# Optimization experiments

Measured on AMD Instinct MI355X. Metric: run time of the kernel, lower is better.

## Reference

```python
import jax, jax.numpy as jnp
import numpy as np

N_NODES = 100000
N_EDGES = 800000
IN_F, H_F, OUT_F = 512, 256, 64
N_EXPERTS = 4  # k = 1


def _normalize_edges(edge_index, n):
    """gcn_norm: add self loops, symmetric D^-1/2 A D^-1/2 edge weights."""
    loop = jnp.arange(n, dtype=edge_index.dtype)
    row = jnp.concatenate([edge_index[0], loop])
    col = jnp.concatenate([edge_index[1], loop])
    w = jnp.ones(row.shape[0], dtype=jnp.float32)
    deg = jax.ops.segment_sum(w, col, num_segments=n)  # in-degree incl. self loop
    dinv = jnp.where(deg > 0, deg ** -0.5, 0.0)
    norm = dinv[row] * w * dinv[col]
    return row, col, norm


def _propagate(x, row, col, norm, n):
    # message x_j * edge_weight, scatter-add at destination col
    msgs = x[row] * norm[:, None]
    return jax.ops.segment_sum(msgs, col, num_segments=n)


def _moe_linear(x, w_gate, expert_w, expert_b):
    # eval-mode noisy top-k gating with k=1: clean logits, top-1, softmax over
    # a single logit -> gate value 1.0 for the selected expert.
    logits = x @ w_gate                         # [N, E]
    idx = jnp.argmax(logits, axis=-1)           # [N]
    gates = jax.nn.one_hot(idx, N_EXPERTS, dtype=x.dtype)  # [N, E]
    y_all = jnp.einsum('ni,eio->neo', x, expert_w) + expert_b[None]  # [N, E, H]
    return jnp.einsum('ne,neo->no', gates, y_all)


def setup_inputs() -> dict:
    key = jax.random.key(0)
    ks = jax.random.split(key, 8)
    x = jax.random.normal(ks[0], (N_NODES, IN_F), dtype=jnp.float32)
    edge_index = jax.random.randint(ks[1], (2, N_EDGES), 0, N_NODES, dtype=jnp.int64)
    w_gate = jax.random.normal(ks[2], (IN_F, N_EXPERTS), dtype=jnp.float32) * 0.05
    expert_w = jax.random.normal(ks[3], (N_EXPERTS, IN_F, H_F), dtype=jnp.float32) * (1.0 / np.sqrt(IN_F))
    expert_b = jnp.zeros((N_EXPERTS, H_F), dtype=jnp.float32)
    bias1 = jnp.zeros((H_F,), dtype=jnp.float32)
    w2 = jax.random.normal(ks[4], (H_F, OUT_F), dtype=jnp.float32) * (1.0 / np.sqrt(H_F))
    bias2 = jnp.zeros((OUT_F,), dtype=jnp.float32)
    return {"x": x, "edge_index": edge_index, "w_gate": w_gate,
            "expert_w": expert_w, "expert_b": expert_b, "bias1": bias1,
            "w2": w2, "bias2": bias2}


def reference(x, edge_index, w_gate, expert_w, expert_b, bias1, w2, bias2):
    n = x.shape[0]
    row, col, norm = _normalize_edges(edge_index, n)
    # conv1: MoE linear -> propagate -> bias
    h = _moe_linear(x, w_gate, expert_w, expert_b)
    h = _propagate(h, row, col, norm, n) + bias1
    h = jax.nn.relu(h)
    # dropout is identity at eval
    # conv2: plain GCNConv
    h = h @ w2
    h = _propagate(h, row, col, norm, n) + bias2
    return jax.nn.log_softmax(h, axis=1)
```

## Files before the change

kernel.cpp:

```cpp
#include <hip/hip_runtime.h>
#include <math.h>

typedef __bf16 bf16x8 __attribute__((ext_vector_type(8)));
typedef float f32x16 __attribute__((ext_vector_type(16)));

__device__ __forceinline__ unsigned short f2bf(float f) {
  union { float f; unsigned int u; } v; v.f = f;
  unsigned int r = (v.u + 0x7FFFu + ((v.u >> 16) & 1u)) >> 16;
  return (unsigned short)r;
}
__device__ __forceinline__ float bf2f(unsigned short u) {
  union { unsigned int u; float f; } v; v.u = ((unsigned int)u) << 16;
  return v.f;
}
__device__ __forceinline__ void bf2x(unsigned int u, float& lo, float& hi) {
  union { unsigned int u; float f; } a, b;
  a.u = u << 16; b.u = u & 0xFFFF0000u;
  lo = a.f; hi = b.f;
}
__device__ __forceinline__ void gload16(const void* g, void* l) {
  __builtin_amdgcn_global_load_lds(
      (__attribute__((address_space(1))) void*)const_cast<void*>(g),
      (__attribute__((address_space(3))) void*)l, 16, 0, 0);
}

__global__ void k_init(int* cnt, int* meta, int N) {
  int i = blockIdx.x * blockDim.x + threadIdx.x;
  if (i < N) cnt[i] = 0;
  if (i < 32) meta[i] = 0;
}

__global__ void k_count(const int* __restrict__ col, int* __restrict__ cnt, int E) {
  int e = blockIdx.x * blockDim.x + threadIdx.x;
  if (e < E) atomicAdd(&cnt[col[e]], 1);
}

__global__ __launch_bounds__(256) void k_scanA(const int* __restrict__ cnt,
                                               int* __restrict__ incl,
                                               int* __restrict__ bsums, int N) {
  __shared__ int s[1024];
  int base = blockIdx.x * 1024;
  #pragma unroll
  for (int t = 0; t < 4; ++t) {
    int i = threadIdx.x + t * 256;
    int idx = base + i;
    s[i] = (idx < N) ? cnt[idx] : 0;
  }
  __syncthreads();
  for (int d = 1; d < 1024; d <<= 1) {
    int v[4];
    #pragma unroll
    for (int t = 0; t < 4; ++t) {
      int i = threadIdx.x + t * 256;
      v[t] = (i >= d) ? s[i - d] : 0;
    }
    __syncthreads();
    #pragma unroll
    for (int t = 0; t < 4; ++t) {
      int i = threadIdx.x + t * 256;
      s[i] += v[t];
    }
    __syncthreads();
  }
  #pragma unroll
  for (int t = 0; t < 4; ++t) {
    int i = threadIdx.x + t * 256;
    int idx = base + i;
    if (idx < N) incl[idx] = s[i];
  }
  if (threadIdx.x == 0) bsums[blockIdx.x] = s[1023];
}

__global__ __launch_bounds__(256) void k_scanB(const int* __restrict__ bsums,
                                               int* __restrict__ boff, int nb) {
  __shared__ int s[1024];
  #pragma unroll
  for (int t = 0; t < 4; ++t) {
    int i = threadIdx.x + t * 256;
    s[i] = (i < nb) ? bsums[i] : 0;
  }
  __syncthreads();
  for (int d = 1; d < 1024; d <<= 1) {
    int v[4];
    #pragma unroll
    for (int t = 0; t < 4; ++t) {
      int i = threadIdx.x + t * 256;
      v[t] = (i >= d) ? s[i - d] : 0;
    }
    __syncthreads();
    #pragma unroll
    for (int t = 0; t < 4; ++t) {
      int i = threadIdx.x + t * 256;
      s[i] += v[t];
    }
    __syncthreads();
  }
  #pragma unroll
  for (int t = 0; t < 4; ++t) {
    int i = threadIdx.x + t * 256;
    if (i < nb) boff[i] = (i == 0) ? 0 : s[i - 1];
  }
}

__global__ void k_scanC(const int* __restrict__ cnt, const int* __restrict__ incl,
                        const int* __restrict__ boff, int* __restrict__ rowptr,
                        int* __restrict__ cursor, float* __restrict__ dinv, int N, int E) {
  int i = blockIdx.x * blockDim.x + threadIdx.x;
  if (i < N) {
    int ex = incl[i] - cnt[i] + boff[i >> 10];
    rowptr[i] = ex;
    cursor[i] = ex;
    dinv[i] = rsqrtf((float)(cnt[i] + 1));
    if (i == 0) rowptr[N] = E;
  }
}

__global__ void k_scatter(const int* __restrict__ row, const int* __restrict__ col,
                          int* __restrict__ cursor, int* __restrict__ csr, int E) {
  int e = blockIdx.x * blockDim.x + threadIdx.x;
  if (e < E) {
    int c = col[e];
    int p = atomicAdd(&cursor[c], 1);
    csr[p] = row[e];
  }
}

__global__ __launch_bounds__(256) void k_gate(const float* __restrict__ x,
                                              const float* __restrict__ wg,
                                              int* __restrict__ eidx,
                                              int* __restrict__ meta,
                                              unsigned short* __restrict__ xb, int N) {
  __shared__ int lhist[4];
  int tid = threadIdx.x;
  if (tid < 4) lhist[tid] = 0;
  __syncthreads();
  int node = blockIdx.x * 16 + (tid >> 4);
  int sl = tid & 15;
  if (node < N) {
    const float* xr = x + (size_t)node * 512;
    unsigned short* xbr = xb + (size_t)node * 512;
    float l0 = 0.f, l1 = 0.f, l2 = 0.f, l3 = 0.f;
    #pragma unroll
    for (int j = 0; j < 8; ++j) {
      int q = sl + 16 * j;
      float4 xv = *(const float4*)(xr + 4 * q);
      ushort4 ov;
      ov.x = f2bf(xv.x); ov.y = f2bf(xv.y); ov.z = f2bf(xv.z); ov.w = f2bf(xv.w);
      *(ushort4*)(xbr + 4 * q) = ov;
      float4 w0 = *(const float4*)(wg + 4 * (4 * q + 0));
      float4 w1 = *(const float4*)(wg + 4 * (4 * q + 1));
      float4 w2 = *(const float4*)(wg + 4 * (4 * q + 2));
      float4 w3 = *(const float4*)(wg + 4 * (4 * q + 3));
      l0 += xv.x * w0.x + xv.y * w1.x + xv.z * w2.x + xv.w * w3.x;
      l1 += xv.x * w0.y + xv.y * w1.y + xv.z * w2.y + xv.w * w3.y;
      l2 += xv.x * w0.z + xv.y * w1.z + xv.z * w2.z + xv.w * w3.z;
      l3 += xv.x * w0.w + xv.y * w1.w + xv.z * w2.w + xv.w * w3.w;
    }
    #pragma unroll
    for (int off = 8; off > 0; off >>= 1) {
      l0 += __shfl_xor(l0, off, 64);
      l1 += __shfl_xor(l1, off, 64);
      l2 += __shfl_xor(l2, off, 64);
      l3 += __shfl_xor(l3, off, 64);
    }
    if (sl == 0) {
      int a = 0; float best = l0;
      if (l1 > best) { best = l1; a = 1; }
      if (l2 > best) { best = l2; a = 2; }
      if (l3 > best) { best = l3; a = 3; }
      eidx[node] = a;
      atomicAdd(&lhist[a], 1);
    }
  }
  __syncthreads();
  if (tid < 4 && lhist[tid] > 0) atomicAdd(&meta[tid], lhist[tid]);
}

__global__ void k_offs(int* meta) {
  if (threadIdx.x == 0 && blockIdx.x == 0) {
    int* hist = meta;
    int* eoff = meta + 4;
    int* toff = meta + 9;
    int* ecur = meta + 14;
    int s = 0, t = 0;
    eoff[0] = 0; toff[0] = 0;
    for (int e = 0; e < 4; ++e) {
      s += hist[e];
      eoff[e + 1] = s;
      t += (hist[e] + 127) / 128;
      toff[e + 1] = t;
      ecur[e] = eoff[e];
    }
  }
}

__global__ __launch_bounds__(256) void k_binscatter(const int* __restrict__ eidx,
                                                    int* __restrict__ meta,
                                                    int* __restrict__ perm, int N) {
  __shared__ int lhist[4];
  __shared__ int lbase[4];
  int tid = threadIdx.x;
  if (tid < 4) lhist[tid] = 0;
  __syncthreads();
  int n = blockIdx.x * 256 + tid;
  int e = 0, lrank = 0;
  bool valid = (n < N);
  if (valid) {
    e = eidx[n];
    lrank = atomicAdd(&lhist[e], 1);
  }
  __syncthreads();
  if (tid < 4) {
    int c = lhist[tid];
    lbase[tid] = (c > 0) ? atomicAdd(&meta[14 + tid], c) : 0;
  }
  __syncthreads();
  if (valid) perm[lbase[e] + lrank] = n;
}

__global__ __launch_bounds__(256) void k_pack(const float* __restrict__ ew,
                                              unsigned short* __restrict__ ewb,
                                              const float* __restrict__ w2,
                                              unsigned short* __restrict__ w2b) {
  int b = blockIdx.x;
  if (b < 256) {
    int n = threadIdx.x;
    int e = b >> 6, kc = b & 63;
    const float* src = ew + ((size_t)e * 512 + (size_t)kc * 8) * 256 + n;
    unsigned short tmp[8];
    #pragma unroll
    for (int ke = 0; ke < 8; ++ke) tmp[ke] = f2bf(src[(size_t)ke * 256]);
    *(uint4*)(ewb + ((size_t)b * 256 + n) * 8) = *(const uint4*)tmp;
  } else {
    int kc = b - 256;
    int n = threadIdx.x;
    if (n < 64) {
      const float* src = w2 + (size_t)kc * 8 * 64 + n;
      unsigned short tmp[8];
      #pragma unroll
      for (int ke = 0; ke < 8; ++ke) tmp[ke] = f2bf(src[(size_t)ke * 64]);
      *(uint4*)(w2b + ((size_t)kc * 64 + n) * 8) = *(const uint4*)tmp;
    }
  }
}

__global__ __launch_bounds__(512, 2) void k_gemm1(const unsigned short* __restrict__ xb,
                                                  const unsigned short* __restrict__ ewb,
                                                  const float* __restrict__ eb,
                                                  const int* __restrict__ perm,
                                                  const int* __restrict__ meta,
                                                  unsigned short* __restrict__ h1) {
  __shared__ __align__(16) unsigned short A_lds[8192];
  __shared__ __align__(16) unsigned short B_lds[16384];
  __shared__ int sperm[128];
  const int* eoff = meta + 4;
  const int* toff = meta + 9;
  int v = blockIdx.x;
  if (v >= toff[4]) return;
  int e = 0;
  while (v >= toff[e + 1]) ++e;
  int m0 = eoff[e] + (v - toff[e]) * 128;
  int mEnd = eoff[e + 1];
  int tid = threadIdx.x;

  if (tid < 128) {
    int m = m0 + tid;
    sperm[tid] = perm[(m < mEnd) ? m : (mEnd - 1)];
  }
  __syncthreads();

  int wave = tid >> 6, lane = tid & 63;
  int wr = wave >> 2, wc = wave & 3;
  int hi = lane >> 5, lo = lane & 31;
  int r128 = tid & 127;

  f32x16 acc[2][2];
  #pragma unroll
  for (int mi = 0; mi < 2; ++mi)
    #pragma unroll
    for (int ni = 0; ni < 2; ++ni)
      #pragma unroll
      for (int r = 0; r < 16; ++r) acc[mi][ni][r] = 0.f;

  const unsigned short* arow = xb + (size_t)sperm[r128] * 512;
  int kclA = tid >> 7;
  const uint4* ebase = (const uint4*)(ewb + (size_t)e * 64 * 2048);

  for (int k0 = 0; k0 < 512; k0 += 64) {
    __syncthreads();
    gload16(arow + k0 + kclA * 8,       &A_lds[((size_t)kclA * 128 + r128) * 8]);
    gload16(arow + k0 + (kclA + 4) * 8, &A_lds[((size_t)(kclA + 4) * 128 + r128) * 8]);
    const uint4* bsrc = ebase + (size_t)(k0 >> 3) * 256;
    gload16(bsrc + tid,        &B_lds[((size_t)0 * 512 + tid) * 8]);
    gload16(bsrc + 512 + tid,  &B_lds[((size_t)1 * 512 + tid) * 8]);
    gload16(bsrc + 1024 + tid, &B_lds[((size_t)2 * 512 + tid) * 8]);
    gload16(bsrc + 1536 + tid, &B_lds[((size_t)3 * 512 + tid) * 8]);
    __syncthreads();
    #pragma unroll
    for (int s = 0; s < 4; ++s) {
      int kcl = s * 2 + hi;
      bf16x8 a0f = *(const bf16x8*)&A_lds[((size_t)kcl * 128 + wr * 64 + lo) * 8];
      bf16x8 a1f = *(const bf16x8*)&A_lds[((size_t)kcl * 128 + wr * 64 + 32 + lo) * 8];
      bf16x8 b0f = *(const bf16x8*)&B_lds[((size_t)kcl * 256 + wc * 64 + lo) * 8];
      bf16x8 b1f = *(const bf16x8*)&B_lds[((size_t)kcl * 256 + wc * 64 + 32 + lo) * 8];
      acc[0][0] = __builtin_amdgcn_mfma_f32_32x32x16_bf16(a0f, b0f, acc[0][0], 0, 0, 0);
      acc[0][1] = __builtin_amdgcn_mfma_f32_32x32x16_bf16(a0f, b1f, acc[0][1], 0, 0, 0);
      acc[1][0] = __builtin_amdgcn_mfma_f32_32x32x16_bf16(a1f, b0f, acc[1][0], 0, 0, 0);
      acc[1][1] = __builtin_amdgcn_mfma_f32_32x32x16_bf16(a1f, b1f, acc[1][1], 0, 0, 0);
    }
  }

  #pragma unroll
  for (int ni = 0; ni < 2; ++ni) {
    int col = wc * 64 + ni * 32 + lo;
    float bias = eb[e * 256 + col];
    #pragma unroll
    for (int mi = 0; mi < 2; ++mi) {
      #pragma unroll
      for (int q = 0; q < 4; ++q) {
        #pragma unroll
        for (int j = 0; j < 4; ++j) {
          int r = j + 8 * q + 4 * hi;
          int lrow = wr * 64 + mi * 32 + r;
          if (m0 + lrow < mEnd) {
            h1[(size_t)sperm[lrow] * 256 + col] = f2bf(acc[mi][ni][q * 4 + j] + bias);
          }
        }
      }
    }
  }
}

__global__ __launch_bounds__(256) void k_prop1(const unsigned short* __restrict__ h1,
                                               const int* __restrict__ rowptr,
                                               const int* __restrict__ csr,
                                               const float* __restrict__ dinv,
                                               const float* __restrict__ bias1,
                                               unsigned short* __restrict__ hrelu, int N) {
  int tid = threadIdx.x;
  int c = blockIdx.x * 8 + (tid >> 5);
  int l = tid & 31;
  if (c >= N) return;
  float dc = dinv[c];
  const uint4* hr = (const uint4*)h1;
  uint4 sv = hr[(size_t)c * 32 + l];
  float slf = dc * dc;
  float a0, a1, a2, a3, a4, a5, a6, a7;
  {
    float lo, hi;
    bf2x(sv.x, lo, hi); a0 = lo * slf; a1 = hi * slf;
    bf2x(sv.y, lo, hi); a2 = lo * slf; a3 = hi * slf;
    bf2x(sv.z, lo, hi); a4 = lo * slf; a5 = hi * slf;
    bf2x(sv.w, lo, hi); a6 = lo * slf; a7 = hi * slf;
  }
  int jb = rowptr[c], je = rowptr[c + 1];
  int j = jb;
  #define ACC8(v, s) { float lo, hi; \
    bf2x((v).x, lo, hi); a0 += lo * (s); a1 += hi * (s); \
    bf2x((v).y, lo, hi); a2 += lo * (s); a3 += hi * (s); \
    bf2x((v).z, lo, hi); a4 += lo * (s); a5 += hi * (s); \
    bf2x((v).w, lo, hi); a6 += lo * (s); a7 += hi * (s); }
  for (; j + 7 < je; j += 8) {
    int r[8];
    #pragma unroll
    for (int t = 0; t < 8; ++t) r[t] = csr[j + t];
    float s[8];
    #pragma unroll
    for (int t = 0; t < 8; ++t) s[t] = dinv[r[t]] * dc;
    uint4 vv[8];
    #pragma unroll
    for (int t = 0; t < 8; ++t) vv[t] = hr[(size_t)r[t] * 32 + l];
    #pragma unroll
    for (int t = 0; t < 8; ++t) ACC8(vv[t], s[t]);
  }
  for (; j + 3 < je; j += 4) {
    int r0 = csr[j], r1 = csr[j + 1], r2 = csr[j + 2], r3 = csr[j + 3];
    float s0 = dinv[r0] * dc, s1 = dinv[r1] * dc, s2 = dinv[r2] * dc, s3 = dinv[r3] * dc;
    uint4 v0 = hr[(size_t)r0 * 32 + l];
    uint4 v1 = hr[(size_t)r1 * 32 + l];
    uint4 v2 = hr[(size_t)r2 * 32 + l];
    uint4 v3 = hr[(size_t)r3 * 32 + l];
    ACC8(v0, s0); ACC8(v1, s1); ACC8(v2, s2); ACC8(v3, s3);
  }
  for (; j < je; ++j) {
    int r = csr[j];
    float s = dinv[r] * dc;
    uint4 v = hr[(size_t)r * 32 + l];
    ACC8(v, s);
  }
  #undef ACC8
  float4 b01 = *(const float4*)(bias1 + l * 8);
  float4 b23 = *(const float4*)(bias1 + l * 8 + 4);
  a0 = fmaxf(a0 + b01.x, 0.f); a1 = fmaxf(a1 + b01.y, 0.f);
  a2 = fmaxf(a2 + b01.z, 0.f); a3 = fmaxf(a3 + b01.w, 0.f);
  a4 = fmaxf(a4 + b23.x, 0.f); a5 = fmaxf(a5 + b23.y, 0.f);
  a6 = fmaxf(a6 + b23.z, 0.f); a7 = fmaxf(a7 + b23.w, 0.f);
  uint4 ov;
  ov.x = ((unsigned int)f2bf(a1) << 16) | f2bf(a0);
  ov.y = ((unsigned int)f2bf(a3) << 16) | f2bf(a2);
  ov.z = ((unsigned int)f2bf(a5) << 16) | f2bf(a4);
  ov.w = ((unsigned int)f2bf(a7) << 16) | f2bf(a6);
  ((uint4*)hrelu)[(size_t)c * 32 + l] = ov;
}

__global__ __launch_bounds__(256, 2) void k_gemm2(const unsigned short* __restrict__ A,
                                                  const unsigned short* __restrict__ w2b,
                                                  unsigned short* __restrict__ h3, int N) {
  __shared__ __align__(16) unsigned short B_lds[16384];
  __shared__ __align__(16) unsigned short A_lds[8192];
  int tid = threadIdx.x;
  int m0 = blockIdx.x * 128;
  #pragma unroll
  for (int it = 0; it < 8; ++it)
    gload16(((const uint4*)w2b) + it * 256 + tid, &B_lds[((size_t)it * 256 + tid) * 8]);

  int wave = tid >> 6, lane = tid & 63;
  int wr = wave >> 1, wc = wave & 1;
  int hi = lane >> 5, lo = lane & 31;

  f32x16 acc[2];
  #pragma unroll
  for (int mi = 0; mi < 2; ++mi)
    #pragma unroll
    for (int r = 0; r < 16; ++r) acc[mi][r] = 0.f;

  int i = tid & 127;
  int row = m0 + i;
  if (row >= N) row = N - 1;
  const unsigned short* arow = A + (size_t)row * 256;
  int kcl0 = tid >> 7;

  for (int k0 = 0; k0 < 256; k0 += 64) {
    __syncthreads();
    #pragma unroll
    for (int t = 0; t < 4; ++t)
      gload16(arow + k0 + (kcl0 + 2 * t) * 8,
              &A_lds[((size_t)(kcl0 + 2 * t) * 128 + i) * 8]);
    __syncthreads();
    #pragma unroll
    for (int s = 0; s < 4; ++s) {
      int kcl = s * 2 + hi;
      bf16x8 a0f = *(const bf16x8*)&A_lds[((size_t)kcl * 128 + wr * 64 + lo) * 8];
      bf16x8 a1f = *(const bf16x8*)&A_lds[((size_t)kcl * 128 + wr * 64 + 32 + lo) * 8];
      bf16x8 bf = *(const bf16x8*)&B_lds[(((size_t)(k0 >> 3) + kcl) * 64 + wc * 32 + lo) * 8];
      acc[0] = __builtin_amdgcn_mfma_f32_32x32x16_bf16(a0f, bf, acc[0], 0, 0, 0);
      acc[1] = __builtin_amdgcn_mfma_f32_32x32x16_bf16(a1f, bf, acc[1], 0, 0, 0);
    }
  }

  int n = wc * 32 + lo;
  #pragma unroll
  for (int mi = 0; mi < 2; ++mi) {
    #pragma unroll
    for (int q = 0; q < 4; ++q) {
      #pragma unroll
      for (int j = 0; j < 4; ++j) {
        int r = j + 8 * q + 4 * hi;
        int orow = m0 + wr * 64 + mi * 32 + r;
        if (orow < N) h3[(size_t)orow * 64 + n] = f2bf(acc[mi][q * 4 + j]);
      }
    }
  }
}

__global__ __launch_bounds__(256) void k_prop2(const unsigned short* __restrict__ h3,
                                               const int* __restrict__ rowptr,
                                               const int* __restrict__ csr,
                                               const float* __restrict__ dinv,
                                               const float* __restrict__ bias2,
                                               float* __restrict__ out, int N) {
  int tid = threadIdx.x;
  int c = blockIdx.x * 32 + (tid >> 3);
  int l = tid & 7;
  if (c >= N) return;
  float dc = dinv[c];
  const uint4* hr = (const uint4*)h3;
  uint4 sv = hr[(size_t)c * 8 + l];
  float slf = dc * dc;
  float a0, a1, a2, a3, a4, a5, a6, a7;
  {
    float lo, hi;
    bf2x(sv.x, lo, hi); a0 = lo * slf; a1 = hi * slf;
    bf2x(sv.y, lo, hi); a2 = lo * slf; a3 = hi * slf;
    bf2x(sv.z, lo, hi); a4 = lo * slf; a5 = hi * slf;
    bf2x(sv.w, lo, hi); a6 = lo * slf; a7 = hi * slf;
  }
  int jb = rowptr[c], je = rowptr[c + 1];
  int j = jb;
  #define ACC8(v, s) { float lo, hi; \
    bf2x((v).x, lo, hi); a0 += lo * (s); a1 += hi * (s); \
    bf2x((v).y, lo, hi); a2 += lo * (s); a3 += hi * (s); \
    bf2x((v).z, lo, hi); a4 += lo * (s); a5 += hi * (s); \
    bf2x((v).w, lo, hi); a6 += lo * (s); a7 += hi * (s); }
  for (; j + 7 < je; j += 8) {
    int r[8];
    #pragma unroll
    for (int t = 0; t < 8; ++t) r[t] = csr[j + t];
    float s[8];
    #pragma unroll
    for (int t = 0; t < 8; ++t) s[t] = dinv[r[t]] * dc;
    uint4 vv[8];
    #pragma unroll
    for (int t = 0; t < 8; ++t) vv[t] = hr[(size_t)r[t] * 8 + l];
    #pragma unroll
    for (int t = 0; t < 8; ++t) ACC8(vv[t], s[t]);
  }
  for (; j + 3 < je; j += 4) {
    int r0 = csr[j], r1 = csr[j + 1], r2 = csr[j + 2], r3 = csr[j + 3];
    float s0 = dinv[r0] * dc, s1 = dinv[r1] * dc, s2 = dinv[r2] * dc, s3 = dinv[r3] * dc;
    uint4 v0 = hr[(size_t)r0 * 8 + l];
    uint4 v1 = hr[(size_t)r1 * 8 + l];
    uint4 v2 = hr[(size_t)r2 * 8 + l];
    uint4 v3 = hr[(size_t)r3 * 8 + l];
    ACC8(v0, s0); ACC8(v1, s1); ACC8(v2, s2); ACC8(v3, s3);
  }
  for (; j < je; ++j) {
    int r = csr[j];
    float s = dinv[r] * dc;
    uint4 v = hr[(size_t)r * 8 + l];
    ACC8(v, s);
  }
  #undef ACC8
  float4 b01 = *(const float4*)(bias2 + l * 8);
  float4 b23 = *(const float4*)(bias2 + l * 8 + 4);
  a0 += b01.x; a1 += b01.y; a2 += b01.z; a3 += b01.w;
  a4 += b23.x; a5 += b23.y; a6 += b23.z; a7 += b23.w;
  float m = fmaxf(fmaxf(fmaxf(a0, a1), fmaxf(a2, a3)), fmaxf(fmaxf(a4, a5), fmaxf(a6, a7)));
  #pragma unroll
  for (int off = 4; off > 0; off >>= 1) m = fmaxf(m, __shfl_xor(m, off, 64));
  float s = expf(a0 - m) + expf(a1 - m) + expf(a2 - m) + expf(a3 - m)
          + expf(a4 - m) + expf(a5 - m) + expf(a6 - m) + expf(a7 - m);
  #pragma unroll
  for (int off = 4; off > 0; off >>= 1) s += __shfl_xor(s, off, 64);
  float ls = m + logf(s);
  float* orow = out + (size_t)c * 64 + l * 8;
  float4 o0 = make_float4(a0 - ls, a1 - ls, a2 - ls, a3 - ls);
  float4 o1 = make_float4(a4 - ls, a5 - ls, a6 - ls, a7 - ls);
  *(float4*)orow = o0;
  *(float4*)(orow + 4) = o1;
}

extern "C" void kernel_launch(void* const* d_in, const int* in_sizes, int n_in,
                              void* d_out, int out_size, void* d_ws, size_t ws_size,
                              hipStream_t stream) {
  const float* x  = (const float*)d_in[0];
  const int*   ei = (const int*)d_in[1];
  const float* wg = (const float*)d_in[2];
  const float* ew = (const float*)d_in[3];
  const float* eb = (const float*)d_in[4];
  const float* b1 = (const float*)d_in[5];
  const float* w2 = (const float*)d_in[6];
  const float* b2 = (const float*)d_in[7];
  float* out = (float*)d_out;

  int N = in_sizes[0] / 512;
  int E = in_sizes[1] / 2;
  const int* row = ei;
  const int* col = ei + E;

  char* p = (char*)d_ws;
  auto alloc = [&](size_t bytes) -> void* {
    void* r = (void*)p;
    p += (bytes + 255) & ~(size_t)255;
    return r;
  };
  int*   cnt    = (int*)alloc((size_t)N * 4);
  int*   rowptr = (int*)alloc((size_t)(N + 1) * 4);
  int*   cursor = (int*)alloc((size_t)N * 4);
  int*   bsums  = (int*)alloc(1024 * 4);
  int*   boff   = (int*)alloc(1024 * 4);
  float* dinv   = (float*)alloc((size_t)N * 4);
  int*   eidx   = (int*)alloc((size_t)N * 4);
  int*   meta   = (int*)alloc(32 * 4);
  int*   perm   = (int*)alloc((size_t)N * 4);
  int*   csr    = (int*)alloc((size_t)E * 4);
  unsigned short* h1    = (unsigned short*)alloc((size_t)N * 256 * 2);
  unsigned short* hrelu = (unsigned short*)alloc((size_t)N * 256 * 2);
  unsigned short* h3    = (unsigned short*)alloc((size_t)N * 64 * 2);
  unsigned short* xb  = (unsigned short*)alloc((size_t)N * 512 * 2);
  unsigned short* ewb = (unsigned short*)alloc((size_t)4 * 512 * 256 * 2);
  unsigned short* w2b = (unsigned short*)alloc((size_t)256 * 64 * 2);

  int nb = (N + 1023) / 1024;

  k_init<<<(N + 255) / 256, 256, 0, stream>>>(cnt, meta, N);
  k_count<<<(E + 255) / 256, 256, 0, stream>>>(col, cnt, E);
  k_scanA<<<nb, 256, 0, stream>>>(cnt, rowptr, bsums, N);
  k_scanB<<<1, 256, 0, stream>>>(bsums, boff, nb);
  k_scanC<<<(N + 255) / 256, 256, 0, stream>>>(cnt, rowptr, boff, rowptr, cursor, dinv, N, E);
  k_scatter<<<(E + 255) / 256, 256, 0, stream>>>(row, col, cursor, csr, E);
  k_pack<<<288, 256, 0, stream>>>(ew, ewb, w2, w2b);
  k_gate<<<(N + 15) / 16, 256, 0, stream>>>(x, wg, eidx, meta, xb, N);
  k_offs<<<1, 64, 0, stream>>>(meta);
  k_binscatter<<<(N + 255) / 256, 256, 0, stream>>>(eidx, meta, perm, N);
  int ntiles = (N + 127) / 128 + 4;
  k_gemm1<<<ntiles, 512, 0, stream>>>(xb, ewb, eb, perm, meta, h1);
  k_prop1<<<(N + 7) / 8, 256, 0, stream>>>(h1, rowptr, csr, dinv, b1, hrelu, N);
  k_gemm2<<<(N + 127) / 128, 256, 0, stream>>>(hrelu, w2b, h3, N);
  k_prop2<<<(N + 31) / 32, 256, 0, stream>>>(h3, rowptr, csr, dinv, b2, out, N);
}
```

Baseline: 397.3 us.

## Fuse count/pack into gate kernel and store source dinv alongside CSR indices

Merges the edge-count atomics and the weight-packing kernel into the gate kernel through block-index ranges, which removes two launches and lets the independent work run concurrently. The CSR now stores (row, dinv[row]) pairs, so the propagation kernels skip a dependent random gather of dinv per edge. In exchange the CSR array doubles in size, and the scatter kernel does an extra dinv gather per edge. The k_gate blocks that take the count and pack paths return before the shared-memory section, which may lengthen that kernel's tail.

```diff
diff --git a/kernel.cpp b/kernel.cpp
--- a/kernel.cpp
+++ b/kernel.cpp
@@ -28,11 +28,6 @@
   int i = blockIdx.x * blockDim.x + threadIdx.x;
   if (i < N) cnt[i] = 0;
   if (i < 32) meta[i] = 0;
-}
-
-__global__ void k_count(const int* __restrict__ col, int* __restrict__ cnt, int E) {
-  int e = blockIdx.x * blockDim.x + threadIdx.x;
-  if (e < E) atomicAdd(&cnt[col[e]], 1);
 }
 
 __global__ __launch_bounds__(256) void k_scanA(const int* __restrict__ cnt,
@@ -116,12 +111,14 @@
 }
 
 __global__ void k_scatter(const int* __restrict__ row, const int* __restrict__ col,
-                          int* __restrict__ cursor, int* __restrict__ csr, int E) {
+                          int* __restrict__ cursor, const float* __restrict__ dinv,
+                          int2* __restrict__ csr2, int E) {
   int e = blockIdx.x * blockDim.x + threadIdx.x;
   if (e < E) {
     int c = col[e];
+    int r = row[e];
     int p = atomicAdd(&cursor[c], 1);
-    csr[p] = row[e];
+    csr2[p] = make_int2(r, __float_as_int(dinv[r]));
   }
 }
 
@@ -129,9 +126,44 @@
                                               const float* __restrict__ wg,
                                               int* __restrict__ eidx,
                                               int* __restrict__ meta,
-                                              unsigned short* __restrict__ xb, int N) {
+                                              unsigned short* __restrict__ xb,
+                                              const int* __restrict__ col,
+                                              int* __restrict__ cnt,
+                                              const float* __restrict__ ew,
+                                              unsigned short* __restrict__ ewb,
+                                              const float* __restrict__ w2,
+                                              unsigned short* __restrict__ w2b,
+                                              int N, int E, int gateB, int cntB) {
+  int tid = threadIdx.x;
+  if (blockIdx.x >= (unsigned)gateB) {
+    int b = blockIdx.x - gateB;
+    if (b < cntB) {
+      int e = b * 256 + tid;
+      if (e < E) atomicAdd(&cnt[col[e]], 1);
+    } else {
+      b -= cntB;
+      if (b < 256) {
+        int n = tid;
+        int eidx2 = b >> 6, kc = b & 63;
+        const float* src = ew + ((size_t)eidx2 * 512 + (size_t)kc * 8) * 256 + n;
+        unsigned short tmp[8];
+        #pragma unroll
+        for (int ke = 0; ke < 8; ++ke) tmp[ke] = f2bf(src[(size_t)ke * 256]);
+        *(uint4*)(ewb + ((size_t)b * 256 + n) * 8) = *(const uint4*)tmp;
+      } else {
+        int kc = b - 256;
+        if (tid < 64) {
+          const float* src = w2 + (size_t)kc * 8 * 64 + tid;
+          unsigned short tmp[8];
+          #pragma unroll
+          for (int ke = 0; ke < 8; ++ke) tmp[ke] = f2bf(src[(size_t)ke * 64]);
+          *(uint4*)(w2b + ((size_t)kc * 64 + tid) * 8) = *(const uint4*)tmp;
+        }
+      }
+    }
+    return;
+  }
   __shared__ int lhist[4];
-  int tid = threadIdx.x;
   if (tid < 4) lhist[tid] = 0;
   __syncthreads();
   int node = blockIdx.x * 16 + (tid >> 4);
@@ -149,12 +181,12 @@
       *(ushort4*)(xbr + 4 * q) = ov;
       float4 w0 = *(const float4*)(wg + 4 * (4 * q + 0));
       float4 w1 = *(const float4*)(wg + 4 * (4 * q + 1));
-      float4 w2 = *(const float4*)(wg + 4 * (4 * q + 2));
+      float4 w2v = *(const float4*)(wg + 4 * (4 * q + 2));
       float4 w3 = *(const float4*)(wg + 4 * (4 * q + 3));
-      l0 += xv.x * w0.x + xv.y * w1.x + xv.z * w2.x + xv.w * w3.x;
-      l1 += xv.x * w0.y + xv.y * w1.y + xv.z * w2.y + xv.w * w3.y;
-      l2 += xv.x * w0.z + xv.y * w1.z + xv.z * w2.z + xv.w * w3.z;
-      l3 += xv.x * w0.w + xv.y * w1.w + xv.z * w2.w + xv.w * w3.w;
+      l0 += xv.x * w0.x + xv.y * w1.x + xv.z * w2v.x + xv.w * w3.x;
+      l1 += xv.x * w0.y + xv.y * w1.y + xv.z * w2v.y + xv.w * w3.y;
+      l2 += xv.x * w0.z + xv.y * w1.z + xv.z * w2v.z + xv.w * w3.z;
+      l3 += xv.x * w0.w + xv.y * w1.w + xv.z * w2v.w + xv.w * w3.w;
     }
     #pragma unroll
     for (int off = 8; off > 0; off >>= 1) {
@@ -216,32 +248,6 @@
   }
   __syncthreads();
   if (valid) perm[lbase[e] + lrank] = n;
-}
-
-__global__ __launch_bounds__(256) void k_pack(const float* __restrict__ ew,
-                                              unsigned short* __restrict__ ewb,
-                                              const float* __restrict__ w2,
-                                              unsigned short* __restrict__ w2b) {
-  int b = blockIdx.x;
-  if (b < 256) {
-    int n = threadIdx.x;
-    int e = b >> 6, kc = b & 63;
-    const float* src = ew + ((size_t)e * 512 + (size_t)kc * 8) * 256 + n;
-    unsigned short tmp[8];
-    #pragma unroll
-    for (int ke = 0; ke < 8; ++ke) tmp[ke] = f2bf(src[(size_t)ke * 256]);
-    *(uint4*)(ewb + ((size_t)b * 256 + n) * 8) = *(const uint4*)tmp;
-  } else {
-    int kc = b - 256;
-    int n = threadIdx.x;
-    if (n < 64) {
-      const float* src = w2 + (size_t)kc * 8 * 64 + n;
-      unsigned short tmp[8];
-      #pragma unroll
-      for (int ke = 0; ke < 8; ++ke) tmp[ke] = f2bf(src[(size_t)ke * 64]);
-      *(uint4*)(w2b + ((size_t)kc * 64 + n) * 8) = *(const uint4*)tmp;
-    }
-  }
 }
 
 __global__ __launch_bounds__(512, 2) void k_gemm1(const unsigned short* __restrict__ xb,
@@ -333,7 +339,7 @@
 
 __global__ __launch_bounds__(256) void k_prop1(const unsigned short* __restrict__ h1,
                                                const int* __restrict__ rowptr,
-                                               const int* __restrict__ csr,
+                                               const int2* __restrict__ csr2,
                                                const float* __restrict__ dinv,
                                                const float* __restrict__ bias1,
                                                unsigned short* __restrict__ hrelu, int N) {
@@ -361,31 +367,32 @@
     bf2x((v).z, lo, hi); a4 += lo * (s); a5 += hi * (s); \
     bf2x((v).w, lo, hi); a6 += lo * (s); a7 += hi * (s); }
   for (; j + 7 < je; j += 8) {
-    int r[8];
-    #pragma unroll
-    for (int t = 0; t < 8; ++t) r[t] = csr[j + t];
-    float s[8];
-    #pragma unroll
-    for (int t = 0; t < 8; ++t) s[t] = dinv[r[t]] * dc;
+    int2 rc[8];
+    #pragma unroll
+    for (int t = 0; t < 8; ++t) rc[t] = csr2[j + t];
     uint4 vv[8];
     #pragma unroll
-    for (int t = 0; t < 8; ++t) vv[t] = hr[(size_t)r[t] * 32 + l];
-    #pragma unroll
-    for (int t = 0; t < 8; ++t) ACC8(vv[t], s[t]);
+    for (int t = 0; t < 8; ++t) vv[t] = hr[(size_t)rc[t].x * 32 + l];
+    #pragma unroll
+    for (int t = 0; t < 8; ++t) {
+      float s = __int_as_float(rc[t].y) * dc;
+      ACC8(vv[t], s);
+    }
   }
   for (; j + 3 < je; j += 4) {
-    int r0 = csr[j], r1 = csr[j + 1], r2 = csr[j + 2], r3 = csr[j + 3];
-    float s0 = dinv[r0] * dc, s1 = dinv[r1] * dc, s2 = dinv[r2] * dc, s3 = dinv[r3] * dc;
-    uint4 v0 = hr[(size_t)r0 * 32 + l];
-    uint4 v1 = hr[(size_t)r1 * 32 + l];
-    uint4 v2 = hr[(size_t)r2 * 32 + l];
-    uint4 v3 = hr[(size_t)r3 * 32 + l];
+    int2 rc0 = csr2[j], rc1 = csr2[j + 1], rc2 = csr2[j + 2], rc3 = csr2[j + 3];
+    uint4 v0 = hr[(size_t)rc0.x * 32 + l];
+    uint4 v1 = hr[(size_t)rc1.x * 32 + l];
+    uint4 v2 = hr[(size_t)rc2.x * 32 + l];
+    uint4 v3 = hr[(size_t)rc3.x * 32 + l];
+    float s0 = __int_as_float(rc0.y) * dc, s1 = __int_as_float(rc1.y) * dc;
+    float s2 = __int_as_float(rc2.y) * dc, s3 = __int_as_float(rc3.y) * dc;
     ACC8(v0, s0); ACC8(v1, s1); ACC8(v2, s2); ACC8(v3, s3);
   }
   for (; j < je; ++j) {
-    int r = csr[j];
-    float s = dinv[r] * dc;
-    uint4 v = hr[(size_t)r * 32 + l];
+    int2 rc = csr2[j];
+    float s = __int_as_float(rc.y) * dc;
+    uint4 v = hr[(size_t)rc.x * 32 + l];
     ACC8(v, s);
   }
   #undef ACC8
@@ -465,7 +472,7 @@
 
 __global__ __launch_bounds__(256) void k_prop2(const unsigned short* __restrict__ h3,
                                                const int* __restrict__ rowptr,
-                                               const int* __restrict__ csr,
+                                               const int2* __restrict__ csr2,
                                                const float* __restrict__ dinv,
                                                const float* __restrict__ bias2,
                                                float* __restrict__ out, int N) {
@@ -493,31 +500,32 @@
     bf2x((v).z, lo, hi); a4 += lo * (s); a5 += hi * (s); \
     bf2x((v).w, lo, hi); a6 += lo * (s); a7 += hi * (s); }
   for (; j + 7 < je; j += 8) {
-    int r[8];
-    #pragma unroll
-    for (int t = 0; t < 8; ++t) r[t] = csr[j + t];
-    float s[8];
-    #pragma unroll
-    for (int t = 0; t < 8; ++t) s[t] = dinv[r[t]] * dc;
+    int2 rc[8];
+    #pragma unroll
+    for (int t = 0; t < 8; ++t) rc[t] = csr2[j + t];
     uint4 vv[8];
     #pragma unroll
-    for (int t = 0; t < 8; ++t) vv[t] = hr[(size_t)r[t] * 8 + l];
-    #pragma unroll
-    for (int t = 0; t < 8; ++t) ACC8(vv[t], s[t]);
+    for (int t = 0; t < 8; ++t) vv[t] = hr[(size_t)rc[t].x * 8 + l];
+    #pragma unroll
+    for (int t = 0; t < 8; ++t) {
+      float s = __int_as_float(rc[t].y) * dc;
+      ACC8(vv[t], s);
+    }
   }
   for (; j + 3 < je; j += 4) {
-    int r0 = csr[j], r1 = csr[j + 1], r2 = csr[j + 2], r3 = csr[j + 3];
-    float s0 = dinv[r0] * dc, s1 = dinv[r1] * dc, s2 = dinv[r2] * dc, s3 = dinv[r3] * dc;
-    uint4 v0 = hr[(size_t)r0 * 8 + l];
-    uint4 v1 = hr[(size_t)r1 * 8 + l];
-    uint4 v2 = hr[(size_t)r2 * 8 + l];
-    uint4 v3 = hr[(size_t)r3 * 8 + l];
+    int2 rc0 = csr2[j], rc1 = csr2[j + 1], rc2 = csr2[j + 2], rc3 = csr2[j + 3];
+    uint4 v0 = hr[(size_t)rc0.x * 8 + l];
+    uint4 v1 = hr[(size_t)rc1.x * 8 + l];
+    uint4 v2 = hr[(size_t)rc2.x * 8 + l];
+    uint4 v3 = hr[(size_t)rc3.x * 8 + l];
+    float s0 = __int_as_float(rc0.y) * dc, s1 = __int_as_float(rc1.y) * dc;
+    float s2 = __int_as_float(rc2.y) * dc, s3 = __int_as_float(rc3.y) * dc;
     ACC8(v0, s0); ACC8(v1, s1); ACC8(v2, s2); ACC8(v3, s3);
   }
   for (; j < je; ++j) {
-    int r = csr[j];
-    float s = dinv[r] * dc;
-    uint4 v = hr[(size_t)r * 8 + l];
+    int2 rc = csr2[j];
+    float s = __int_as_float(rc.y) * dc;
+    uint4 v = hr[(size_t)rc.x * 8 + l];
     ACC8(v, s);
   }
   #undef ACC8
@@ -573,7 +581,7 @@
   int*   eidx   = (int*)alloc((size_t)N * 4);
   int*   meta   = (int*)alloc(32 * 4);
   int*   perm   = (int*)alloc((size_t)N * 4);
-  int*   csr    = (int*)alloc((size_t)E * 4);
+  int2*  csr2   = (int2*)alloc((size_t)E * 8);
   unsigned short* h1    = (unsigned short*)alloc((size_t)N * 256 * 2);
   unsigned short* hrelu = (unsigned short*)alloc((size_t)N * 256 * 2);
   unsigned short* h3    = (unsigned short*)alloc((size_t)N * 64 * 2);
@@ -582,20 +590,21 @@
   unsigned short* w2b = (unsigned short*)alloc((size_t)256 * 64 * 2);
 
   int nb = (N + 1023) / 1024;
+  int gateB = (N + 15) / 16;
+  int cntB = (E + 255) / 256;
 
   k_init<<<(N + 255) / 256, 256, 0, stream>>>(cnt, meta, N);
-  k_count<<<(E + 255) / 256, 256, 0, stream>>>(col, cnt, E);
+  k_gate<<<gateB + cntB + 288, 256, 0, stream>>>(x, wg, eidx, meta, xb, col, cnt,
+                                                 ew, ewb, w2, w2b, N, E, gateB, cntB);
   k_scanA<<<nb, 256, 0, stream>>>(cnt, rowptr, bsums, N);
   k_scanB<<<1, 256, 0, stream>>>(bsums, boff, nb);
   k_scanC<<<(N + 255) / 256, 256, 0, stream>>>(cnt, rowptr, boff, rowptr, cursor, dinv, N, E);
-  k_scatter<<<(E + 255) / 256, 256, 0, stream>>>(row, col, cursor, csr, E);
-  k_pack<<<288, 256, 0, stream>>>(ew, ewb, w2, w2b);
-  k_gate<<<(N + 15) / 16, 256, 0, stream>>>(x, wg, eidx, meta, xb, N);
+  k_scatter<<<(E + 255) / 256, 256, 0, stream>>>(row, col, cursor, dinv, csr2, E);
   k_offs<<<1, 64, 0, stream>>>(meta);
   k_binscatter<<<(N + 255) / 256, 256, 0, stream>>>(eidx, meta, perm, N);
   int ntiles = (N + 127) / 128 + 4;
   k_gemm1<<<ntiles, 512, 0, stream>>>(xb, ewb, eb, perm, meta, h1);
-  k_prop1<<<(N + 7) / 8, 256, 0, stream>>>(h1, rowptr, csr, dinv, b1, hrelu, N);
+  k_prop1<<<(N + 7) / 8, 256, 0, stream>>>(h1, rowptr, csr2, dinv, b1, hrelu, N);
   k_gemm2<<<(N + 127) / 128, 256, 0, stream>>>(hrelu, w2b, h3, N);
-  k_prop2<<<(N + 31) / 32, 256, 0, stream>>>(h3, rowptr, csr, dinv, b2, out, N);
-}
+  k_prop2<<<(N + 31) / 32, 256, 0, stream>>>(h3, rowptr, csr2, dinv, b2, out, N);
+}
```

Result: faster. 366.5 us (-7.7%).
